# Performance work log

Measured on AMD Instinct MI355X. Metric: run time of the kernel, lower is better.

The kernel has to match this reference:

```python
import jax, jax.numpy as jnp
import numpy as np

D_MODEL = 1024
NHEAD = 16
D_K = D_MODEL // NHEAD


def setup_inputs() -> dict:
    key = jax.random.key(0)
    ks = jax.random.split(key, 12)
    B, S = 1, 4096
    s = 1.0 / np.sqrt(D_MODEL)
    inp = {
        "query": jax.random.normal(ks[0], (B, S, D_MODEL), jnp.float32),
        "key": jax.random.normal(ks[1], (B, S, D_MODEL), jnp.float32),
        "value": jax.random.normal(ks[2], (B, S, D_MODEL), jnp.float32),
        "W_q": jax.random.normal(ks[3], (D_MODEL, D_MODEL), jnp.float32) * s,
        "b_q": jnp.zeros((D_MODEL,), jnp.float32),
        "W_k": jax.random.normal(ks[4], (D_MODEL, D_MODEL), jnp.float32) * s,
        "b_k": jnp.zeros((D_MODEL,), jnp.float32),
        "W_v": jax.random.normal(ks[5], (D_MODEL, D_MODEL), jnp.float32) * s,
        "b_v": jnp.zeros((D_MODEL,), jnp.float32),
        "W_o": jax.random.normal(ks[6], (D_MODEL, D_MODEL), jnp.float32) * s,
        "b_o": jnp.zeros((D_MODEL,), jnp.float32),
    }
    return inp


def reference(query, key, value, W_q, b_q, W_k, b_k, W_v, b_v, W_o, b_o):
    B, S, _ = query.shape
    # linear projections (torch Linear: x @ W.T + b)
    Q = query @ W_q.T + b_q
    K = key @ W_k.T + b_k
    V = value @ W_v.T + b_v
    # split heads: [B, S, D] -> [B, H, S, d_k]
    Q = Q.reshape(B, S, NHEAD, D_K).transpose(0, 2, 1, 3)
    K = K.reshape(B, S, NHEAD, D_K).transpose(0, 2, 1, 3)
    V = V.reshape(B, S, NHEAD, D_K).transpose(0, 2, 1, 3)
    # scaled dot-product attention (materializes [B,H,S,S] like original)
    scores = jnp.einsum("bhqd,bhkd->bhqk", Q, K) / jnp.sqrt(jnp.float32(D_K))
    weights = jax.nn.softmax(scores, axis=-1)
    attn = jnp.einsum("bhqk,bhkd->bhqd", weights, V)
    # combine heads: [B, H, S, d_k] -> [B, S, D]
    attn = attn.transpose(0, 2, 1, 3).reshape(B, S, D_MODEL)
    return attn @ W_o.T + b_o
```

## Files before the change

### kernel.cpp

```cpp
#include <hip/hip_runtime.h>
#include <hip/hip_bf16.h>
#include <type_traits>

constexpr int SEQ = 4096;
constexpr int DMODEL = 1024;
constexpr int NH = 16;
constexpr int DKH = 64;
constexpr float SCALE = 0.125f;
constexpr float SCALE2 = 0.125f * 1.4426950408889634f;

typedef __bf16 bf16x8 __attribute__((ext_vector_type(8)));
typedef __bf16 bf16x4 __attribute__((ext_vector_type(4)));
typedef float f32x4 __attribute__((ext_vector_type(4)));
typedef float f32x16 __attribute__((ext_vector_type(16)));
typedef unsigned int u32x4 __attribute__((ext_vector_type(4)));
union W8 { u32x4 u; bf16x8 v; };

__device__ inline void store_c(__hip_bfloat16* p, float v) { *p = __float2bfloat16(v); }
__device__ inline void store_c(float* p, float v) { *p = v; }

typedef const void __attribute__((address_space(1)))* gas_ptr;
typedef void __attribute__((address_space(3)))* las_ptr;
__device__ inline void load_lds_16B(const void* g, void* l) {
  __builtin_amdgcn_global_load_lds((gas_ptr)g, (las_ptr)l, 16, 0, 0);
}

__device__ inline unsigned pack2(float a, float b) {
  union { __bf16 h[2]; unsigned u; } p;
  p.h[0] = (__bf16)a; p.h[1] = (__bf16)b;
  return p.u;
}

__device__ inline void st8(__hip_bfloat16* buf, int row, int col, bf16x8 v) {
  *(bf16x8*)(buf + row * 64 + (col ^ ((row & 7) << 3))) = v;
}
__device__ inline bf16x8 ld8(const __hip_bfloat16* buf, int row, int col) {
  return *(const bf16x8*)(buf + row * 64 + (col ^ ((row & 7) << 3)));
}

__global__ __launch_bounds__(256)
void cvt_all(const float* __restrict__ q, const float* __restrict__ k,
             const float* __restrict__ v, const float* __restrict__ wq,
             const float* __restrict__ wk, const float* __restrict__ wv,
             const float* __restrict__ wo,
             __bf16* __restrict__ Xq, __bf16* __restrict__ Xk,
             __bf16* __restrict__ Xv, __bf16* __restrict__ Wqb,
             __bf16* __restrict__ Wkb, __bf16* __restrict__ Wvb,
             __bf16* __restrict__ Wob) {
  const int b = blockIdx.x;
  const float* src; __bf16* dst; size_t base;
  if      (b < 2048) { src = q;  dst = Xq;  base = b; }
  else if (b < 4096) { src = k;  dst = Xk;  base = b - 2048; }
  else if (b < 6144) { src = v;  dst = Xv;  base = b - 4096; }
  else if (b < 6656) { src = wq; dst = Wqb; base = b - 6144; }
  else if (b < 7168) { src = wk; dst = Wkb; base = b - 6656; }
  else if (b < 7680) { src = wv; dst = Wvb; base = b - 7168; }
  else               { src = wo; dst = Wob; base = b - 7680; }
  const size_t i = (base * 256 + threadIdx.x) * 8;
  const float4 a = *(const float4*)(src + i);
  const float4 c = *(const float4*)(src + i + 4);
  bf16x8 r = {(__bf16)a.x, (__bf16)a.y, (__bf16)a.z, (__bf16)a.w,
              (__bf16)c.x, (__bf16)c.y, (__bf16)c.z, (__bf16)c.w};
  *(bf16x8*)(dst + i) = r;
}

constexpr int BK = 64;

template <typename TC, bool TRANS_C>
__global__ __launch_bounds__(256)
void gemm128(const __bf16* __restrict__ A,
             const __bf16* __restrict__ W,
             const float* __restrict__ bias,
             TC* __restrict__ C,
             float out_scale) {
  __shared__ alignas(16) __bf16 As[128][64];
  __shared__ alignas(16) __bf16 Ws[64][64];

  const int t = threadIdx.x;
  const int lane = t & 63;
  const int w = t >> 6;
  const int wr = w >> 1;
  const int wc = w & 1;
  const int col = lane & 15;
  const int quad = lane >> 4;

  const int L = blockIdx.x + 16 * blockIdx.y;
  const int xcd = L & 7;
  const int c = L >> 3;
  const int m_blk = (xcd * 4 + (c >> 4)) * 128;
  const int n_blk = (c & 15) * 64;

  const int srow = t >> 3;
  const int scol = (t & 7) * 8;

  f32x4 acc[4][2] = {};

  for (int k0 = 0; k0 < DMODEL; k0 += BK) {
    __syncthreads();
    #pragma unroll
    for (int p = 0; p < 4; ++p)
      load_lds_16B(A + (size_t)(m_blk + p * 32 + srow) * DMODEL + k0 + scol,
                   &As[p * 32 + srow][scol]);
    #pragma unroll
    for (int p = 0; p < 2; ++p)
      load_lds_16B(W + (size_t)(n_blk + p * 32 + srow) * DMODEL + k0 + scol,
                   &Ws[p * 32 + srow][scol]);
    __syncthreads();

    #pragma unroll
    for (int kh = 0; kh < BK; kh += 32) {
      bf16x8 af[4], bfr[2];
      #pragma unroll
      for (int at = 0; at < 4; ++at)
        af[at] = *(const bf16x8*)&As[wr * 64 + at * 16 + col][kh + quad * 8];
      #pragma unroll
      for (int bt = 0; bt < 2; ++bt)
        bfr[bt] = *(const bf16x8*)&Ws[wc * 32 + bt * 16 + col][kh + quad * 8];
      #pragma unroll
      for (int at = 0; at < 4; ++at)
        #pragma unroll
        for (int bt = 0; bt < 2; ++bt)
          acc[at][bt] = __builtin_amdgcn_mfma_f32_16x16x32_bf16(
              af[at], bfr[bt], acc[at][bt], 0, 0, 0);
    }
  }

  #pragma unroll
  for (int at = 0; at < 4; ++at) {
    #pragma unroll
    for (int bt = 0; bt < 2; ++bt) {
      const int n = n_blk + wc * 32 + bt * 16 + col;
      const float b = bias[n];
      #pragma unroll
      for (int i = 0; i < 4; ++i) {
        const int m = m_blk + wr * 64 + at * 16 + quad * 4 + i;
        const float v = (acc[at][bt][i] + b) * out_scale;
        if constexpr (TRANS_C) store_c(&C[(size_t)n * SEQ + m], v);
        else                   store_c(&C[(size_t)m * DMODEL + n], v);
      }
    }
  }
}

__global__ __launch_bounds__(256)
void gemm_qkv(const __bf16* __restrict__ Xq, const __bf16* __restrict__ Xk,
              const __bf16* __restrict__ Xv, const __bf16* __restrict__ Wq,
              const __bf16* __restrict__ Wk, const __bf16* __restrict__ Wv,
              const float* __restrict__ bq, const float* __restrict__ bk,
              const float* __restrict__ bv,
              __hip_bfloat16* __restrict__ Cq, __hip_bfloat16* __restrict__ Ck,
              __hip_bfloat16* __restrict__ Cv) {
  __shared__ alignas(16) __bf16 As[128][64];
  __shared__ alignas(16) __bf16 Ws[64][64];

  const int L = blockIdx.x + 16 * (blockIdx.y + 32 * blockIdx.z);
  const int xcd = L & 7;
  const int cc = L >> 3;
  const int z = cc / 64;
  const int c2 = cc & 63;
  const int m_blk = (xcd * 4 + (c2 >> 4)) * 128;
  const int n_blk = (c2 & 15) * 64;

  const __bf16* A = (z == 0) ? Xq : (z == 1) ? Xk : Xv;
  const __bf16* W = (z == 0) ? Wq : (z == 1) ? Wk : Wv;
  const float* bias = (z == 0) ? bq : (z == 1) ? bk : bv;
  __hip_bfloat16* C = (z == 0) ? Cq : (z == 1) ? Ck : Cv;
  const float out_scale = (z == 0) ? SCALE2 : 1.0f;

  const int t = threadIdx.x;
  const int lane = t & 63;
  const int w = t >> 6;
  const int wr = w >> 1;
  const int wc = w & 1;
  const int col = lane & 15;
  const int quad = lane >> 4;

  const int srow = t >> 3;
  const int scol = (t & 7) * 8;

  f32x4 acc[4][2] = {};

  for (int k0 = 0; k0 < DMODEL; k0 += BK) {
    __syncthreads();
    #pragma unroll
    for (int p = 0; p < 4; ++p)
      load_lds_16B(A + (size_t)(m_blk + p * 32 + srow) * DMODEL + k0 + scol,
                   &As[p * 32 + srow][scol]);
    #pragma unroll
    for (int p = 0; p < 2; ++p)
      load_lds_16B(W + (size_t)(n_blk + p * 32 + srow) * DMODEL + k0 + scol,
                   &Ws[p * 32 + srow][scol]);
    __syncthreads();

    #pragma unroll
    for (int kh = 0; kh < BK; kh += 32) {
      bf16x8 af[4], bfr[2];
      #pragma unroll
      for (int at = 0; at < 4; ++at)
        af[at] = *(const bf16x8*)&As[wr * 64 + at * 16 + col][kh + quad * 8];
      #pragma unroll
      for (int bt = 0; bt < 2; ++bt)
        bfr[bt] = *(const bf16x8*)&Ws[wc * 32 + bt * 16 + col][kh + quad * 8];
      #pragma unroll
      for (int at = 0; at < 4; ++at)
        #pragma unroll
        for (int bt = 0; bt < 2; ++bt)
          acc[at][bt] = __builtin_amdgcn_mfma_f32_16x16x32_bf16(
              af[at], bfr[bt], acc[at][bt], 0, 0, 0);
    }
  }

  #pragma unroll
  for (int at = 0; at < 4; ++at) {
    #pragma unroll
    for (int bt = 0; bt < 2; ++bt) {
      const int n = n_blk + wc * 32 + bt * 16 + col;
      const float b = bias[n];
      #pragma unroll
      for (int i = 0; i < 4; ++i) {
        const int m = m_blk + wr * 64 + at * 16 + quad * 4 + i;
        const float v = (acc[at][bt][i] + b) * out_scale;
        if (z == 2) C[(size_t)n * SEQ + m] = __float2bfloat16(v);
        else        C[(size_t)m * DMODEL + n] = __float2bfloat16(v);
      }
    }
  }
}

constexpr int LDK = 72;

template <typename TA, typename TC, bool TRANS_C>
__global__ __launch_bounds__(256)
void gemm_tiled(const TA* __restrict__ A,
                const float* __restrict__ W,
                const float* __restrict__ bias,
                TC* __restrict__ C,
                float out_scale) {
  __shared__ alignas(16) __bf16 As[128][LDK];
  __shared__ alignas(16) __bf16 Ws[64][LDK];

  const int t = threadIdx.x;
  const int lane = t & 63;
  const int w = t >> 6;
  const int wr = w >> 1;
  const int wc = w & 1;
  const int col = lane & 15;
  const int quad = lane >> 4;
  const int m_blk = blockIdx.y * 128;
  const int n_blk = blockIdx.x * 64;

  f32x4 acc[4][2] = {};

  for (int k0 = 0; k0 < DMODEL; k0 += BK) {
    __syncthreads();
    if constexpr (std::is_same<TA, float>::value) {
      #pragma unroll
      for (int p = 0; p < 8; ++p) {
        const int r = p * 16 + (t >> 4);
        const int c = (t & 15) * 4;
        const float4 v =
            *(const float4*)(A + (size_t)(m_blk + r) * DMODEL + k0 + c);
        bf16x4 b = {(__bf16)v.x, (__bf16)v.y, (__bf16)v.z, (__bf16)v.w};
        *(bf16x4*)&As[r][c] = b;
      }
    } else {
      #pragma unroll
      for (int p = 0; p < 4; ++p) {
        const int r = p * 32 + (t >> 3);
        const int c = (t & 7) * 8;
        *(bf16x8*)&As[r][c] =
            *(const bf16x8*)((const __bf16*)A + (size_t)(m_blk + r) * DMODEL + k0 + c);
      }
    }
    #pragma unroll
    for (int p = 0; p < 4; ++p) {
      const int r = p * 16 + (t >> 4);
      const int c = (t & 15) * 4;
      const float4 v =
          *(const float4*)(W + (size_t)(n_blk + r) * DMODEL + k0 + c);
      bf16x4 b = {(__bf16)v.x, (__bf16)v.y, (__bf16)v.z, (__bf16)v.w};
      *(bf16x4*)&Ws[r][c] = b;
    }
    __syncthreads();

    #pragma unroll
    for (int kh = 0; kh < BK; kh += 32) {
      bf16x8 af[4], bfr[2];
      #pragma unroll
      for (int at = 0; at < 4; ++at)
        af[at] = *(const bf16x8*)&As[wr * 64 + at * 16 + col][kh + quad * 8];
      #pragma unroll
      for (int bt = 0; bt < 2; ++bt)
        bfr[bt] = *(const bf16x8*)&Ws[wc * 32 + bt * 16 + col][kh + quad * 8];
      #pragma unroll
      for (int at = 0; at < 4; ++at)
        #pragma unroll
        for (int bt = 0; bt < 2; ++bt)
          acc[at][bt] = __builtin_amdgcn_mfma_f32_16x16x32_bf16(
              af[at], bfr[bt], acc[at][bt], 0, 0, 0);
    }
  }

  #pragma unroll
  for (int at = 0; at < 4; ++at) {
    #pragma unroll
    for (int bt = 0; bt < 2; ++bt) {
      const int n = n_blk + wc * 32 + bt * 16 + col;
      const float b = bias[n];
      #pragma unroll
      for (int i = 0; i < 4; ++i) {
        const int m = m_blk + wr * 64 + at * 16 + quad * 4 + i;
        const float v = (acc[at][bt][i] + b) * out_scale;
        if constexpr (TRANS_C) store_c(&C[(size_t)n * SEQ + m], v);
        else                   store_c(&C[(size_t)m * DMODEL + n], v);
      }
    }
  }
}

__global__ __launch_bounds__(256, 4)
void flash_attn_splitN(const __hip_bfloat16* __restrict__ Q,
                       const __hip_bfloat16* __restrict__ K,
                       const __hip_bfloat16* __restrict__ Vt,
                       __hip_bfloat16* __restrict__ Op0,
                       __hip_bfloat16* __restrict__ Op1,
                       __hip_bfloat16* __restrict__ Op2,
                       __hip_bfloat16* __restrict__ Op3,
                       float* __restrict__ lsum_g, int head0) {
  __shared__ alignas(16) __hip_bfloat16 kt[64 * 64];
  __shared__ alignas(16) __hip_bfloat16 vtt[64 * 64];

  const int t = threadIdx.x;
  const int lane = t & 63;
  const int w = t >> 6;
  const int head = head0 + blockIdx.y;
  const int q0 = blockIdx.x * 128;
  const int z = blockIdx.z;
  const int nz = gridDim.z;
  const int l31 = lane & 31;
  const int hl = lane >> 5;

  __hip_bfloat16* O = (z == 0) ? Op0 : (z == 1) ? Op1 : (z == 2) ? Op2 : Op3;

  bf16x8 qf[4];
  {
    const __hip_bfloat16* qp =
        Q + (size_t)(q0 + w * 32 + l31) * DMODEL + head * DKH + hl * 8;
    #pragma unroll
    for (int db = 0; db < 4; ++db) qf[db] = *(const bf16x8*)(qp + db * 16);
  }

  f32x16 acc_o[2] = {};
  float lsa = 0.f, lsb = 0.f;

  const int sr = t >> 2;
  const int sc = (t & 3) * 16;
  const int seg = SEQ / nz;
  const int NT = seg / 64;
  const int kbeg = z * seg;

  const __hip_bfloat16* kgp = K + (size_t)(kbeg + sr) * DMODEL + head * DKH + sc;
  const __hip_bfloat16* vgp = Vt + (size_t)(head * DKH + sr) * SEQ + kbeg + sc;

  bf16x8 kr0 = *(const bf16x8*)kgp;
  bf16x8 kr1 = *(const bf16x8*)(kgp + 8);
  bf16x8 vr0 = *(const bf16x8*)vgp;
  bf16x8 vr1 = *(const bf16x8*)(vgp + 8);

  for (int ti = 0; ti < NT; ++ti) {
    __syncthreads();
    st8(kt, sr, sc, kr0);  st8(kt, sr, sc + 8, kr1);
    st8(vtt, sr, sc, vr0); st8(vtt, sr, sc + 8, vr1);
    __syncthreads();

    if (ti + 1 < NT) {
      const __hip_bfloat16* kn = kgp + (size_t)(ti + 1) * 64 * DMODEL;
      const __hip_bfloat16* vn = vgp + (ti + 1) * 64;
      kr0 = *(const bf16x8*)kn; kr1 = *(const bf16x8*)(kn + 8);
      vr0 = *(const bf16x8*)vn; vr1 = *(const bf16x8*)(vn + 8);
    }

    bf16x8 pa[4];
    #pragma unroll
    for (int kb = 0; kb < 2; ++kb) {
      f32x16 s = {};
      __builtin_amdgcn_s_setprio(1);
      #pragma unroll
      for (int db = 0; db < 4; ++db) {
        const bf16x8 kf = ld8(kt, kb * 32 + l31, db * 16 + hl * 8);
        s = __builtin_amdgcn_mfma_f32_32x32x16_bf16(kf, qf[db], s, 0, 0, 0);
      }
      __builtin_amdgcn_s_setprio(0);
      unsigned wp[8];
      #pragma unroll
      for (int i = 0; i < 8; ++i) {
        const float p0 = __builtin_amdgcn_exp2f(s[2 * i]);
        const float p1 = __builtin_amdgcn_exp2f(s[2 * i + 1]);
        lsa += p0; lsb += p1;
        wp[i] = pack2(p0, p1);
      }
      #pragma unroll
      for (int b = 0; b < 2; ++b) {
        unsigned a0 = wp[4 * b + 0], a2 = wp[4 * b + 2];
        unsigned a1 = wp[4 * b + 1], a3 = wp[4 * b + 3];
        asm("v_permlane32_swap_b32 %0, %1" : "+v"(a0), "+v"(a2));
        asm("v_permlane32_swap_b32 %0, %1" : "+v"(a1), "+v"(a3));
        W8 u;
        u.u[0] = a0; u.u[1] = a1; u.u[2] = a2; u.u[3] = a3;
        pa[kb * 2 + b] = u.v;
      }
    }

    __builtin_amdgcn_s_setprio(1);
    #pragma unroll
    for (int kq = 0; kq < 4; ++kq)
      #pragma unroll
      for (int db = 0; db < 2; ++db) {
        const bf16x8 vb = ld8(vtt, db * 32 + l31, kq * 16 + hl * 8);
        acc_o[db] = __builtin_amdgcn_mfma_f32_32x32x16_bf16(
            pa[kq], vb, acc_o[db], 0, 0, 0);
      }
    __builtin_amdgcn_s_setprio(0);
  }

  float lsumq = lsa + lsb;
  lsumq += __shfl_xor(lsumq, 32);
  if (lane < 32)
    lsum_g[((size_t)z * NH + head) * SEQ + q0 + w * 32 + lane] = lsumq;

  #pragma unroll
  for (int db = 0; db < 2; ++db) {
    #pragma unroll
    for (int r = 0; r < 16; ++r) {
      const int qr = q0 + w * 32 + (r & 3) + 8 * (r >> 2) + 4 * hl;
      const int cidx = head * DKH + db * 32 + l31;
      O[(size_t)qr * DMODEL + cidx] = __float2bfloat16(acc_o[db][r]);
    }
  }
}

__global__ __launch_bounds__(256)
void attn_combine(const __hip_bfloat16* __restrict__ Op0,
                  const __hip_bfloat16* __restrict__ Op1,
                  const __hip_bfloat16* __restrict__ Op2,
                  const __hip_bfloat16* __restrict__ Op3,
                  const float* __restrict__ ls,
                  __hip_bfloat16* __restrict__ Ao, int nz) {
  const size_t i = ((size_t)blockIdx.x * 256 + threadIdx.x) * 8;
  const int qrow = (int)(i >> 10);
  const int h = (int)((i & 1023) >> 6);
  float lsum = ls[(size_t)h * SEQ + qrow] +
               ls[(size_t)(NH + h) * SEQ + qrow];
  const bf16x8 a = *(const bf16x8*)(Op0 + i);
  const bf16x8 b = *(const bf16x8*)(Op1 + i);
  float s[8];
  #pragma unroll
  for (int j = 0; j < 8; ++j) s[j] = (float)a[j] + (float)b[j];
  if (nz == 4) {
    lsum += ls[(size_t)(2 * NH + h) * SEQ + qrow] +
            ls[(size_t)(3 * NH + h) * SEQ + qrow];
    const bf16x8 c = *(const bf16x8*)(Op2 + i);
    const bf16x8 d = *(const bf16x8*)(Op3 + i);
    #pragma unroll
    for (int j = 0; j < 8; ++j) s[j] += (float)c[j] + (float)d[j];
  }
  const float inv = 1.f / lsum;
  bf16x8 r;
  #pragma unroll
  for (int j = 0; j < 8; ++j) r[j] = (__bf16)(s[j] * inv);
  *(bf16x8*)(Ao + i) = r;
}

constexpr int LDP = 72;
constexpr float SHIFT = 8.0f;

__global__ __launch_bounds__(256)
void flash_attn_mono(const __hip_bfloat16* __restrict__ Q,
                     const __hip_bfloat16* __restrict__ K,
                     const __hip_bfloat16* __restrict__ Vt,
                     __hip_bfloat16* __restrict__ O) {
  __shared__ alignas(16) __hip_bfloat16 kt[64][LDP];
  __shared__ alignas(16) __hip_bfloat16 vtt[DKH][LDP];
  __shared__ alignas(16) __hip_bfloat16 plT[4][32][LDP];

  const int t = threadIdx.x;
  const int lane = t & 63;
  const int w = t >> 6;
  const int h = blockIdx.y;
  const int q0 = blockIdx.x * 128;
  const int col = lane & 15;
  const int quad = lane >> 4;

  bf16x8 qf[2][2];
  #pragma unroll
  for (int rg = 0; rg < 2; ++rg) {
    const __hip_bfloat16* qptr =
        Q + (size_t)(q0 + w * 32 + rg * 16 + col) * DMODEL + h * DKH + quad * 8;
    qf[rg][0] = *(const bf16x8*)qptr;
    qf[rg][1] = *(const bf16x8*)(qptr + 32);
  }

  f32x4 acc_o[2][4] = {};
  float lsumq[2] = {0.f, 0.f};
  const int sr = t >> 2;
  const int sc = (t & 3) * 16;

  for (int k0 = 0; k0 < SEQ; k0 += 64) {
    __syncthreads();
    const __hip_bfloat16* kg = K + (size_t)(k0 + sr) * DMODEL + h * DKH + sc;
    *(bf16x8*)&kt[sr][sc]     = *(const bf16x8*)kg;
    *(bf16x8*)&kt[sr][sc + 8] = *(const bf16x8*)(kg + 8);
    const __hip_bfloat16* vg = Vt + (size_t)(h * DKH + sr) * SEQ + k0 + sc;
    *(bf16x8*)&vtt[sr][sc]     = *(const bf16x8*)vg;
    *(bf16x8*)&vtt[sr][sc + 8] = *(const bf16x8*)(vg + 8);
    __syncthreads();

    #pragma unroll
    for (int jt = 0; jt < 4; ++jt) {
      const bf16x8 kf0 = *(const bf16x8*)&kt[jt * 16 + col][quad * 8];
      const bf16x8 kf1 = *(const bf16x8*)&kt[jt * 16 + col][quad * 8 + 32];
      #pragma unroll
      for (int rg = 0; rg < 2; ++rg) {
        f32x4 zz = {0.f, 0.f, 0.f, 0.f};
        zz = __builtin_amdgcn_mfma_f32_16x16x32_bf16(kf0, qf[rg][0], zz, 0, 0, 0);
        zz = __builtin_amdgcn_mfma_f32_16x16x32_bf16(kf1, qf[rg][1], zz, 0, 0, 0);
        bf16x4 pk;
        #pragma unroll
        for (int r = 0; r < 4; ++r) {
          const float p = __expf(zz[r] - SHIFT);
          lsumq[rg] += p;
          pk[r] = (__bf16)p;
        }
        *(bf16x4*)&plT[w][rg * 16 + col][jt * 16 + quad * 4] = pk;
      }
    }

    bf16x8 pa[2][2];
    #pragma unroll
    for (int rg = 0; rg < 2; ++rg) {
      pa[rg][0] = *(const bf16x8*)&plT[w][rg * 16 + col][quad * 8];
      pa[rg][1] = *(const bf16x8*)&plT[w][rg * 16 + col][quad * 8 + 32];
    }
    #pragma unroll
    for (int jt = 0; jt < 4; ++jt) {
      const bf16x8 vb0 = *(const bf16x8*)&vtt[jt * 16 + col][quad * 8];
      const bf16x8 vb1 = *(const bf16x8*)&vtt[jt * 16 + col][quad * 8 + 32];
      #pragma unroll
      for (int rg = 0; rg < 2; ++rg) {
        acc_o[rg][jt] = __builtin_amdgcn_mfma_f32_16x16x32_bf16(
            pa[rg][0], vb0, acc_o[rg][jt], 0, 0, 0);
        acc_o[rg][jt] = __builtin_amdgcn_mfma_f32_16x16x32_bf16(
            pa[rg][1], vb1, acc_o[rg][jt], 0, 0, 0);
      }
    }
  }

  #pragma unroll
  for (int rg = 0; rg < 2; ++rg) {
    lsumq[rg] += __shfl_xor(lsumq[rg], 16);
    lsumq[rg] += __shfl_xor(lsumq[rg], 32);
  }
  float invr[2][4];
  #pragma unroll
  for (int rg = 0; rg < 2; ++rg)
    #pragma unroll
    for (int r = 0; r < 4; ++r)
      invr[rg][r] = 1.f / __shfl(lsumq[rg], quad * 4 + r);

  #pragma unroll
  for (int rg = 0; rg < 2; ++rg) {
    #pragma unroll
    for (int jt = 0; jt < 4; ++jt) {
      #pragma unroll
      for (int r = 0; r < 4; ++r) {
        const int qr = q0 + w * 32 + rg * 16 + quad * 4 + r;
        const int c = h * DKH + jt * 16 + col;
        O[(size_t)qr * DMODEL + c] = __float2bfloat16(acc_o[rg][jt][r] * invr[rg][r]);
      }
    }
  }
}

extern "C" void kernel_launch(void* const* d_in, const int* in_sizes, int n_in,
                              void* d_out, int out_size, void* d_ws, size_t ws_size,
                              hipStream_t stream) {
  const float* query = (const float*)d_in[0];
  const float* key   = (const float*)d_in[1];
  const float* value = (const float*)d_in[2];
  const float* W_q   = (const float*)d_in[3];
  const float* b_q   = (const float*)d_in[4];
  const float* W_k   = (const float*)d_in[5];
  const float* b_k   = (const float*)d_in[6];
  const float* W_v   = (const float*)d_in[7];
  const float* b_v   = (const float*)d_in[8];
  const float* W_o   = (const float*)d_in[9];
  const float* b_o   = (const float*)d_in[10];

  float* out = (float*)d_out;
  const size_t mat = (size_t)SEQ * DMODEL;
  const size_t MB = 1024 * 1024;

  char* ws = (char*)d_ws;
  __hip_bfloat16* Qp = (__hip_bfloat16*)d_out;
  __hip_bfloat16* Kp = (__hip_bfloat16*)ws;
  __hip_bfloat16* Vt = Kp + mat;

  dim3 gblock(256);

  if (ws_size >= 40 * MB) {
    __bf16* Xq  = (__bf16*)((char*)d_out + 8 * MB);
    __bf16* Xk  = (__bf16*)(ws + 16 * MB);
    __bf16* Xv  = (__bf16*)(ws + 24 * MB);
    __bf16* Wqb = (__bf16*)(ws + 32 * MB);
    __bf16* Wkb = (__bf16*)(ws + 34 * MB);
    __bf16* Wvb = (__bf16*)(ws + 36 * MB);
    __bf16* Wob = (__bf16*)(ws + 38 * MB);
    __hip_bfloat16* Op0 = (__hip_bfloat16*)(ws + 16 * MB);
    __hip_bfloat16* Op1 = (__hip_bfloat16*)(ws + 24 * MB);
    __hip_bfloat16* Op2 = (__hip_bfloat16*)((char*)d_out + 8 * MB);
    __hip_bfloat16* Op3 = (__hip_bfloat16*)(ws + 40 * MB);
    float* lsum = (float*)(ws + 33 * MB);
    __hip_bfloat16* Ao = (__hip_bfloat16*)(ws + 16 * MB);

    const int nz = (ws_size >= 48 * MB) ? 4 : 2;

    hipLaunchKernelGGL(cvt_all, dim3(8192), gblock, 0, stream,
                       query, key, value, W_q, W_k, W_v, W_o,
                       Xq, Xk, Xv, Wqb, Wkb, Wvb, Wob);

    dim3 qkvgrid(DMODEL / 64, SEQ / 128, 3);
    hipLaunchKernelGGL(gemm_qkv, qkvgrid, gblock, 0, stream,
                       Xq, Xk, Xv, Wqb, Wkb, Wvb, b_q, b_k, b_v,
                       Qp, Kp, Vt);

    dim3 agrid(SEQ / 128, NH / 2, nz);
    hipLaunchKernelGGL(flash_attn_splitN, agrid, gblock, 0, stream,
                       Qp, Kp, Vt, Op0, Op1, Op2, Op3, lsum, 0);
    hipLaunchKernelGGL(flash_attn_splitN, agrid, gblock, 0, stream,
                       Qp, Kp, Vt, Op0, Op1, Op2, Op3, lsum, NH / 2);
    hipLaunchKernelGGL(attn_combine, dim3(2048), gblock, 0, stream,
                       Op0, Op1, Op2, Op3, lsum, Ao, nz);

    dim3 ogrid(DMODEL / 64, SEQ / 128);
    hipLaunchKernelGGL((gemm128<float, false>), ogrid, gblock, 0, stream,
                       (const __bf16*)Ao, Wob, b_o, out, 1.0f);
  } else {
    __hip_bfloat16* Ao = Qp + mat;
    float* Cw = (float*)d_ws;
    dim3 fgrid(DMODEL / 64, SEQ / 128);
    hipLaunchKernelGGL((gemm_tiled<float, __hip_bfloat16, false>), fgrid, gblock,
                       0, stream, query, W_q, b_q, Qp, SCALE);
    hipLaunchKernelGGL((gemm_tiled<float, __hip_bfloat16, false>), fgrid, gblock,
                       0, stream, key, W_k, b_k, Kp, 1.0f);
    hipLaunchKernelGGL((gemm_tiled<float, __hip_bfloat16, true>), fgrid, gblock,
                       0, stream, value, W_v, b_v, Vt, 1.0f);
    dim3 agrid(SEQ / 128, NH);
    hipLaunchKernelGGL(flash_attn_mono, agrid, gblock, 0, stream, Qp, Kp, Vt, Ao);
    hipLaunchKernelGGL((gemm_tiled<__hip_bfloat16, float, false>), fgrid, gblock,
                       0, stream, Ao, W_o, b_o, Cw, 1.0f);
    hipMemcpyAsync(out, Cw, mat * sizeof(float), hipMemcpyDeviceToDevice, stream);
  }
}
```

Before: 285.8 us.

## Swizzle GEMM LDS tiles with XOR and merge two attention launches into one

The GEMM kernels now load global columns in XOR-permuted order into LDS and read fragments back through a matching XOR on the column index. The goal is to spread the fragment reads across LDS banks and avoid bank conflicts. Separately, the two half-head flash-attention launches become a single launch over all 16 heads, which removes a launch gap and fills the GPU with one larger grid. The swizzle needs the load and read permutations to agree exactly, or the results will be wrong.

```diff
diff --git a/kernel.cpp b/kernel.cpp
--- a/kernel.cpp
+++ b/kernel.cpp
@@ -91,7 +91,9 @@
   const int n_blk = (c & 15) * 64;
 
   const int srow = t >> 3;
-  const int scol = (t & 7) * 8;
+  const int scol_l = (t & 7) * 8;
+  const int scol_g = ((t & 7) ^ (srow & 7)) * 8;
+  const int rsw = (col & 7) * 8;
 
   f32x4 acc[4][2] = {};
 
@@ -99,12 +101,12 @@
     __syncthreads();
     #pragma unroll
     for (int p = 0; p < 4; ++p)
-      load_lds_16B(A + (size_t)(m_blk + p * 32 + srow) * DMODEL + k0 + scol,
-                   &As[p * 32 + srow][scol]);
+      load_lds_16B(A + (size_t)(m_blk + p * 32 + srow) * DMODEL + k0 + scol_g,
+                   &As[p * 32 + srow][scol_l]);
     #pragma unroll
     for (int p = 0; p < 2; ++p)
-      load_lds_16B(W + (size_t)(n_blk + p * 32 + srow) * DMODEL + k0 + scol,
-                   &Ws[p * 32 + srow][scol]);
+      load_lds_16B(W + (size_t)(n_blk + p * 32 + srow) * DMODEL + k0 + scol_g,
+                   &Ws[p * 32 + srow][scol_l]);
     __syncthreads();
 
     #pragma unroll
@@ -112,10 +114,10 @@
       bf16x8 af[4], bfr[2];
       #pragma unroll
       for (int at = 0; at < 4; ++at)
-        af[at] = *(const bf16x8*)&As[wr * 64 + at * 16 + col][kh + quad * 8];
+        af[at] = *(const bf16x8*)&As[wr * 64 + at * 16 + col][(kh + quad * 8) ^ rsw];
       #pragma unroll
       for (int bt = 0; bt < 2; ++bt)
-        bfr[bt] = *(const bf16x8*)&Ws[wc * 32 + bt * 16 + col][kh + quad * 8];
+        bfr[bt] = *(const bf16x8*)&Ws[wc * 32 + bt * 16 + col][(kh + quad * 8) ^ rsw];
       #pragma unroll
       for (int at = 0; at < 4; ++at)
         #pragma unroll
@@ -176,7 +178,9 @@
   const int quad = lane >> 4;
 
   const int srow = t >> 3;
-  const int scol = (t & 7) * 8;
+  const int scol_l = (t & 7) * 8;
+  const int scol_g = ((t & 7) ^ (srow & 7)) * 8;
+  const int rsw = (col & 7) * 8;
 
   f32x4 acc[4][2] = {};
 
@@ -184,12 +188,12 @@
     __syncthreads();
     #pragma unroll
     for (int p = 0; p < 4; ++p)
-      load_lds_16B(A + (size_t)(m_blk + p * 32 + srow) * DMODEL + k0 + scol,
-                   &As[p * 32 + srow][scol]);
+      load_lds_16B(A + (size_t)(m_blk + p * 32 + srow) * DMODEL + k0 + scol_g,
+                   &As[p * 32 + srow][scol_l]);
     #pragma unroll
     for (int p = 0; p < 2; ++p)
-      load_lds_16B(W + (size_t)(n_blk + p * 32 + srow) * DMODEL + k0 + scol,
-                   &Ws[p * 32 + srow][scol]);
+      load_lds_16B(W + (size_t)(n_blk + p * 32 + srow) * DMODEL + k0 + scol_g,
+                   &Ws[p * 32 + srow][scol_l]);
     __syncthreads();
 
     #pragma unroll
@@ -197,10 +201,10 @@
       bf16x8 af[4], bfr[2];
       #pragma unroll
       for (int at = 0; at < 4; ++at)
-        af[at] = *(const bf16x8*)&As[wr * 64 + at * 16 + col][kh + quad * 8];
+        af[at] = *(const bf16x8*)&As[wr * 64 + at * 16 + col][(kh + quad * 8) ^ rsw];
       #pragma unroll
       for (int bt = 0; bt < 2; ++bt)
-        bfr[bt] = *(const bf16x8*)&Ws[wc * 32 + bt * 16 + col][kh + quad * 8];
+        bfr[bt] = *(const bf16x8*)&Ws[wc * 32 + bt * 16 + col][(kh + quad * 8) ^ rsw];
       #pragma unroll
       for (int at = 0; at < 4; ++at)
         #pragma unroll
@@ -326,14 +330,14 @@
                        __hip_bfloat16* __restrict__ Op1,
                        __hip_bfloat16* __restrict__ Op2,
                        __hip_bfloat16* __restrict__ Op3,
-                       float* __restrict__ lsum_g, int head0) {
+                       float* __restrict__ lsum_g) {
   __shared__ alignas(16) __hip_bfloat16 kt[64 * 64];
   __shared__ alignas(16) __hip_bfloat16 vtt[64 * 64];
 
   const int t = threadIdx.x;
   const int lane = t & 63;
   const int w = t >> 6;
-  const int head = head0 + blockIdx.y;
+  const int head = blockIdx.y;
   const int q0 = blockIdx.x * 128;
   const int z = blockIdx.z;
   const int nz = gridDim.z;
@@ -633,11 +637,9 @@
                        Xq, Xk, Xv, Wqb, Wkb, Wvb, b_q, b_k, b_v,
                        Qp, Kp, Vt);
 
-    dim3 agrid(SEQ / 128, NH / 2, nz);
+    dim3 agrid(SEQ / 128, NH, nz);
     hipLaunchKernelGGL(flash_attn_splitN, agrid, gblock, 0, stream,
-                       Qp, Kp, Vt, Op0, Op1, Op2, Op3, lsum, 0);
-    hipLaunchKernelGGL(flash_attn_splitN, agrid, gblock, 0, stream,
-                       Qp, Kp, Vt, Op0, Op1, Op2, Op3, lsum, NH / 2);
+                       Qp, Kp, Vt, Op0, Op1, Op2, Op3, lsum);
     hipLaunchKernelGGL(attn_combine, dim3(2048), gblock, 0, stream,
                        Op0, Op1, Op2, Op3, lsum, Ao, nz);
 
```

After: 266.1 us (median of 2 runs). 6.9% less time.
